# Performance work log

Measured on AMD Instinct MI355X. Metric: run time of the kernel, lower is better.

Reference implementation:

```python
import jax, jax.numpy as jnp
import numpy as np

B, N, D = 8, 512, 512
H = 8
DK = D // H  # 64 per-channel attention maps


def setup_inputs() -> dict:
    key = jax.random.key(0)
    k1, k2, k3 = jax.random.split(key, 3)
    inputs = jax.random.normal(k1, (B, N, D), dtype=jnp.float32)
    W_qkv = jax.random.normal(k2, (D, 3 * DK), dtype=jnp.float32) * 0.02
    W_o = jax.random.normal(k3, (DK, D), dtype=jnp.float32) * 0.02
    return {"inputs": inputs, "W_qkv": W_qkv, "W_o": W_o}


def reference(inputs, W_qkv, W_o):
    d_k = W_qkv.shape[1] // 3
    QKV = inputs @ W_qkv                      # (B, N, 3*d_k)
    Q = QKV[:, :, 0 * d_k:1 * d_k]
    K = QKV[:, :, 1 * d_k:2 * d_k]
    V = QKV[:, :, 2 * d_k:3 * d_k]
    scale = 1.0 / jnp.sqrt(jnp.asarray(d_k, dtype=QKV.dtype))
    # per-channel (head_dim=1) attention, batched over the d_k channels
    S = jnp.einsum('bnc,bmc->bcnm', Q, K) * scale   # (B, d_k, N, N)
    A = jax.nn.softmax(S, axis=-1)
    SA = jnp.einsum('bcnm,bmc->bnc', A, V)          # (B, N, d_k)
    return SA @ W_o                                 # (B, N, D)
```

## Files before the change

kernel.cpp:

```cpp
#include <hip/hip_runtime.h>
#include <math.h>

#define BB 8
#define NN 512
#define DD 512
#define DKK 64
#define NC 192
#define CHN (BB * DKK * NN)
#define XEL (BB * NN * DD)
#define WEL (NC * DD)
#define NFRAG_X (XEL / 8)
#define NFRAG_W (WEL / 8)
#define NJ 20

typedef short s8v   __attribute__((ext_vector_type(8)));
typedef float f32x4 __attribute__((ext_vector_type(4)));
typedef unsigned short ushort;

static __device__ __forceinline__ ushort bf16_rne(float f) {
    unsigned u = __float_as_uint(f);
    unsigned r = 0x7FFFu + ((u >> 16) & 1u);
    return (ushort)((u + r) >> 16);
}
static __device__ __forceinline__ float bf16_f32(ushort h) {
    return __uint_as_float(((unsigned)h) << 16);
}

__constant__ float c_invfact[NJ] = {
    1.0f, 1.0f, 0.5f, 1.6666667e-1f, 4.1666668e-2f, 8.3333338e-3f,
    1.3888889e-3f, 1.9841270e-4f, 2.4801588e-5f, 2.7557319e-6f,
    2.7557319e-7f, 2.5052108e-8f, 2.0876757e-9f, 1.6059044e-10f,
    1.1470746e-11f, 7.6471637e-13f, 4.7794773e-14f, 2.8114572e-15f,
    1.5619207e-16f, 8.2206352e-18f};

__global__ __launch_bounds__(256) void prep(const float* __restrict__ X,
                                            const float* __restrict__ W,
                                            ushort* __restrict__ Xfh,
                                            ushort* __restrict__ Xfl,
                                            ushort* __restrict__ Wfh,
                                            ushort* __restrict__ Wfl) {
    const int gtid = blockIdx.x * 256 + threadIdx.x;
    if (gtid < NFRAG_X) {
        const int st   = gtid >> 10;
        const int ks   = (gtid >> 6) & 15;
        const int lane = gtid & 63;
        const int lm   = lane & 15;
        const int quad = lane >> 4;
        const int row  = st * 16 + lm;
        const int k0   = ks * 32 + quad * 8;
        const float4 xa = *(const float4*)(X + (size_t)row * DD + k0);
        const float4 xb = *(const float4*)(X + (size_t)row * DD + k0 + 4);
        const float xe[8] = {xa.x, xa.y, xa.z, xa.w, xb.x, xb.y, xb.z, xb.w};
        s8v h, l;
        #pragma unroll
        for (int e = 0; e < 8; ++e) {
            const ushort hh = bf16_rne(xe[e]);
            h[e] = (short)hh;
            l[e] = (short)bf16_rne(xe[e] - bf16_f32(hh));
        }
        *(s8v*)(Xfh + (size_t)gtid * 8) = h;
        *(s8v*)(Xfl + (size_t)gtid * 8) = l;
    } else {
        const int widx = gtid - NFRAG_X;
        if (widx < NFRAG_W) {
            const int ct   = widx >> 10;
            const int ks   = (widx >> 6) & 15;
            const int lane = widx & 63;
            const int lm   = lane & 15;
            const int quad = lane >> 4;
            const int chan = ct * 16 + lm;
            const int k0   = ks * 32 + quad * 8;
            s8v h, l;
            #pragma unroll
            for (int e = 0; e < 8; ++e) {
                const float w = W[(size_t)(k0 + e) * NC + chan];
                const ushort hh = bf16_rne(w);
                h[e] = (short)hh;
                l[e] = (short)bf16_rne(w - bf16_f32(hh));
            }
            *(s8v*)(Wfh + (size_t)widx * 8) = h;
            *(s8v*)(Wfl + (size_t)widx * 8) = l;
        }
    }
}

__global__ __launch_bounds__(256) void qkv_mfma(const ushort* __restrict__ Xfh,
                                                const ushort* __restrict__ Xfl,
                                                const ushort* __restrict__ Wfh,
                                                const ushort* __restrict__ Wfl,
                                                float* __restrict__ qkv) {
    const int widx = blockIdx.x * 4 + (threadIdx.x >> 6);
    const int st   = widx / 12;
    const int ct   = widx - st * 12;
    const int lane = threadIdx.x & 63;

    const ushort* ax_h = Xfh + ((size_t)(st * 16) * 64 + lane) * 8;
    const ushort* ax_l = Xfl + ((size_t)(st * 16) * 64 + lane) * 8;
    const ushort* bw_h = Wfh + ((size_t)(ct * 16) * 64 + lane) * 8;
    const ushort* bw_l = Wfl + ((size_t)(ct * 16) * 64 + lane) * 8;

    f32x4 acc = {0.f, 0.f, 0.f, 0.f};

    #pragma unroll 4
    for (int ks = 0; ks < 16; ++ks) {
        const size_t off = (size_t)ks * 512;
        const s8v ah = *(const s8v*)(ax_h + off);
        const s8v al = *(const s8v*)(ax_l + off);
        const s8v bh = *(const s8v*)(bw_h + off);
        const s8v bl = *(const s8v*)(bw_l + off);
        acc = __builtin_amdgcn_mfma_f32_16x16x32_bf16(ah, bh, acc, 0, 0, 0);
        acc = __builtin_amdgcn_mfma_f32_16x16x32_bf16(ah, bl, acc, 0, 0, 0);
        acc = __builtin_amdgcn_mfma_f32_16x16x32_bf16(al, bh, acc, 0, 0, 0);
    }

    const int lm   = lane & 15;
    const int quad = lane >> 4;
    const int chan = ct * 16 + lm;
    const int which = chan >> 6;
    const int c     = chan & 63;
    const int seq0  = st * 16 + quad * 4;
    const int b     = seq0 >> 9;
    const int n0    = seq0 & 511;
    const float4 v = {acc[0], acc[1], acc[2], acc[3]};
    *(float4*)(qkv + (size_t)which * CHN + ((size_t)(b * DKK + c)) * NN + n0) = v;
}

__global__ __launch_bounds__(256) void attn_taylor(const float* __restrict__ qkv,
                                                   float* __restrict__ sa_t) {
    __shared__ float red[4][2 * NJ];
    __shared__ float coef[2 * NJ];

    const int tid = threadIdx.x;
    const size_t chan = (size_t)blockIdx.x * NN;
    const float* qp = qkv + chan;
    const float* kp = qkv + CHN + chan;
    const float* vp = qkv + 2 * CHN + chan;

    const float k0 = kp[tid], k1 = kp[tid + 256];
    const float v0 = vp[tid], v1 = vp[tid + 256];

    float m[2 * NJ];
    float p0 = 1.f, p1 = 1.f;
    #pragma unroll
    for (int j = 0; j < NJ; ++j) {
        m[j]      = fmaf(p0, v0, p1 * v1);
        m[NJ + j] = p0 + p1;
        p0 *= k0;
        p1 *= k1;
    }

    #pragma unroll
    for (int j = 0; j < 2 * NJ; ++j) {
        float s = m[j];
        #pragma unroll
        for (int off = 32; off > 0; off >>= 1)
            s += __shfl_down(s, off, 64);
        m[j] = s;
    }
    if ((tid & 63) == 0) {
        #pragma unroll
        for (int j = 0; j < 2 * NJ; ++j) red[tid >> 6][j] = m[j];
    }
    __syncthreads();
    if (tid < 2 * NJ) {
        const int jj = (tid < NJ) ? tid : tid - NJ;
        coef[tid] = (red[0][tid] + red[1][tid] + red[2][tid] + red[3][tid]) *
                    c_invfact[jj];
    }
    __syncthreads();

    float c[2 * NJ];
    #pragma unroll
    for (int j = 0; j < 2 * NJ; ++j) c[j] = coef[j];

    #pragma unroll
    for (int r = 0; r < 2; ++r) {
        const float t = qp[tid + r * 256] * 0.125f;
        float P = c[NJ - 1];
        float Q = c[2 * NJ - 1];
        #pragma unroll
        for (int j = NJ - 2; j >= 0; --j) {
            P = fmaf(P, t, c[j]);
            Q = fmaf(Q, t, c[NJ + j]);
        }
        sa_t[chan + tid + r * 256] = P / Q;
    }
}

__global__ __launch_bounds__(256) void out_gemm(const float* __restrict__ sa_t,
                                                const float* __restrict__ Wo,
                                                float* __restrict__ out) {
    __shared__ float As[64][68];
    __shared__ float Bs[64][68];

    const int tid  = threadIdx.x;
    const int row0 = blockIdx.x * 64;
    const int d0   = blockIdx.y * 64;
    const int b    = row0 >> 9;
    const int n0   = row0 & 511;

    const int f  = tid & 15;
    const int r0 = tid >> 4;
    #pragma unroll
    for (int rr = 0; rr < 4; ++rr) {
        const int cidx = r0 + rr * 16;
        *(float4*)&As[cidx][4 * f] =
            *(const float4*)(sa_t + (size_t)(b * DKK + cidx) * NN + n0 + 4 * f);
        *(float4*)&Bs[cidx][4 * f] =
            *(const float4*)(Wo + (size_t)cidx * DD + d0 + 4 * f);
    }
    __syncthreads();

    const int tc = tid & 15;
    const int tr = tid >> 4;
    float acc[4][4] = {};
    #pragma unroll 8
    for (int k = 0; k < DKK; ++k) {
        const float4 a  = *(const float4*)&As[k][4 * tr];
        const float4 bv = *(const float4*)&Bs[k][4 * tc];
        const float av[4] = {a.x, a.y, a.z, a.w};
        const float be[4] = {bv.x, bv.y, bv.z, bv.w};
        #pragma unroll
        for (int i = 0; i < 4; ++i)
            #pragma unroll
            for (int j = 0; j < 4; ++j)
                acc[i][j] = fmaf(av[i], be[j], acc[i][j]);
    }

    float* op = out + ((size_t)(b * NN + n0)) * DD + d0;
    #pragma unroll
    for (int i = 0; i < 4; ++i) {
        const float4 v = {acc[i][0], acc[i][1], acc[i][2], acc[i][3]};
        *(float4*)(op + (size_t)(4 * tr + i) * DD + 4 * tc) = v;
    }
}

extern "C" void kernel_launch(void* const* d_in, const int* in_sizes, int n_in,
                              void* d_out, int out_size, void* d_ws, size_t ws_size,
                              hipStream_t stream) {
    const float* X    = (const float*)d_in[0];
    const float* Wqkv = (const float*)d_in[1];
    const float* Wo   = (const float*)d_in[2];
    float* out = (float*)d_out;

    float*  qkv  = (float*)d_ws;
    float*  sa_t = qkv + (size_t)3 * CHN;
    ushort* Xfh  = (ushort*)(sa_t + CHN);
    ushort* Xfl  = Xfh + (size_t)XEL;
    ushort* Wfh  = Xfl + (size_t)XEL;
    ushort* Wfl  = Wfh + (size_t)WEL;

    prep<<<dim3((NFRAG_X + NFRAG_W + 255) / 256), 256, 0, stream>>>(
        X, Wqkv, Xfh, Xfl, Wfh, Wfl);
    qkv_mfma<<<dim3(768), 256, 0, stream>>>(Xfh, Xfl, Wfh, Wfl, qkv);
    attn_taylor<<<dim3(BB * DKK), 256, 0, stream>>>(qkv, sa_t);
    out_gemm<<<dim3(64, 8), 256, 0, stream>>>(sa_t, Wo, out);
}
```

Measured before the change: 89.91 us.

## Move output projection to split-bf16 MFMA and remap QKV blocks per XCD

The fp32 LDS-tiled output GEMM is replaced with an MFMA kernel using hi/lo bf16 splits (three products per k-step). The attention kernel now writes its result directly in the MFMA fragment layout, and W_o is converted to fragments in the prep kernel. The QKV GEMM block index is also remapped so each XCD handles a contiguous range of sequence tiles, which should improve L2 locality. In exchange, the attention kernel does scattered 2-byte stores, and the output kernel writes with a less coalesced pattern (per-lane scalar stores strided by DD).

```diff
diff --git a/kernel.cpp b/kernel.cpp
--- a/kernel.cpp
+++ b/kernel.cpp
@@ -9,8 +9,11 @@
 #define CHN (BB * DKK * NN)
 #define XEL (BB * NN * DD)
 #define WEL (NC * DD)
+#define WOEL (DKK * DD)
+#define SAEL (BB * NN * DKK)
 #define NFRAG_X (XEL / 8)
 #define NFRAG_W (WEL / 8)
+#define NFRAG_WO (WOEL / 8)
 #define NJ 20
 
 typedef short s8v   __attribute__((ext_vector_type(8)));
@@ -35,10 +38,13 @@
 
 __global__ __launch_bounds__(256) void prep(const float* __restrict__ X,
                                             const float* __restrict__ W,
+                                            const float* __restrict__ Wo,
                                             ushort* __restrict__ Xfh,
                                             ushort* __restrict__ Xfl,
                                             ushort* __restrict__ Wfh,
-                                            ushort* __restrict__ Wfl) {
+                                            ushort* __restrict__ Wfl,
+                                            ushort* __restrict__ Woh,
+                                            ushort* __restrict__ Wol) {
     const int gtid = blockIdx.x * 256 + threadIdx.x;
     if (gtid < NFRAG_X) {
         const int st   = gtid >> 10;
@@ -60,27 +66,48 @@
         }
         *(s8v*)(Xfh + (size_t)gtid * 8) = h;
         *(s8v*)(Xfl + (size_t)gtid * 8) = l;
-    } else {
-        const int widx = gtid - NFRAG_X;
-        if (widx < NFRAG_W) {
-            const int ct   = widx >> 10;
-            const int ks   = (widx >> 6) & 15;
-            const int lane = widx & 63;
-            const int lm   = lane & 15;
-            const int quad = lane >> 4;
-            const int chan = ct * 16 + lm;
-            const int k0   = ks * 32 + quad * 8;
-            s8v h, l;
-            #pragma unroll
-            for (int e = 0; e < 8; ++e) {
-                const float w = W[(size_t)(k0 + e) * NC + chan];
-                const ushort hh = bf16_rne(w);
-                h[e] = (short)hh;
-                l[e] = (short)bf16_rne(w - bf16_f32(hh));
-            }
-            *(s8v*)(Wfh + (size_t)widx * 8) = h;
-            *(s8v*)(Wfl + (size_t)widx * 8) = l;
+        return;
+    }
+    const int widx = gtid - NFRAG_X;
+    if (widx < NFRAG_W) {
+        const int ct   = widx >> 10;
+        const int ks   = (widx >> 6) & 15;
+        const int lane = widx & 63;
+        const int lm   = lane & 15;
+        const int quad = lane >> 4;
+        const int chan = ct * 16 + lm;
+        const int k0   = ks * 32 + quad * 8;
+        s8v h, l;
+        #pragma unroll
+        for (int e = 0; e < 8; ++e) {
+            const float w = W[(size_t)(k0 + e) * NC + chan];
+            const ushort hh = bf16_rne(w);
+            h[e] = (short)hh;
+            l[e] = (short)bf16_rne(w - bf16_f32(hh));
         }
+        *(s8v*)(Wfh + (size_t)widx * 8) = h;
+        *(s8v*)(Wfl + (size_t)widx * 8) = l;
+        return;
+    }
+    const int fi = widx - NFRAG_W;
+    if (fi < NFRAG_WO) {
+        const int lane = fi & 63;
+        const int ks   = (fi >> 6) & 1;
+        const int dt   = fi >> 7;
+        const int lm   = lane & 15;
+        const int quad = lane >> 4;
+        const int d    = dt * 16 + lm;
+        s8v h, l;
+        #pragma unroll
+        for (int e = 0; e < 8; ++e) {
+            const int c = ks * 32 + quad * 8 + e;
+            const float w = Wo[(size_t)c * DD + d];
+            const ushort hh = bf16_rne(w);
+            h[e] = (short)hh;
+            l[e] = (short)bf16_rne(w - bf16_f32(hh));
+        }
+        *(s8v*)(Woh + (size_t)fi * 8) = h;
+        *(s8v*)(Wol + (size_t)fi * 8) = l;
     }
 }
 
@@ -89,9 +116,12 @@
                                                 const ushort* __restrict__ Wfh,
                                                 const ushort* __restrict__ Wfl,
                                                 float* __restrict__ qkv) {
-    const int widx = blockIdx.x * 4 + (threadIdx.x >> 6);
-    const int st   = widx / 12;
-    const int ct   = widx - st * 12;
+    const int xcd  = blockIdx.x & 7;
+    const int grp  = blockIdx.x >> 3;
+    const int stl  = grp / 3;
+    const int part = grp - stl * 3;
+    const int st   = xcd * 32 + stl;
+    const int ct   = part * 4 + (threadIdx.x >> 6);
     const int lane = threadIdx.x & 63;
 
     const ushort* ax_h = Xfh + ((size_t)(st * 16) * 64 + lane) * 8;
@@ -113,9 +143,9 @@
         acc = __builtin_amdgcn_mfma_f32_16x16x32_bf16(al, bh, acc, 0, 0, 0);
     }
 
-    const int lm   = lane & 15;
-    const int quad = lane >> 4;
-    const int chan = ct * 16 + lm;
+    const int lm    = lane & 15;
+    const int quad  = lane >> 4;
+    const int chan  = ct * 16 + lm;
     const int which = chan >> 6;
     const int c     = chan & 63;
     const int seq0  = st * 16 + quad * 4;
@@ -126,7 +156,8 @@
 }
 
 __global__ __launch_bounds__(256) void attn_taylor(const float* __restrict__ qkv,
-                                                   float* __restrict__ sa_t) {
+                                                   ushort* __restrict__ SAh,
+                                                   ushort* __restrict__ SAl) {
     __shared__ float red[4][2 * NJ];
     __shared__ float coef[2 * NJ];
 
@@ -173,9 +204,16 @@
     #pragma unroll
     for (int j = 0; j < 2 * NJ; ++j) c[j] = coef[j];
 
+    const int b  = blockIdx.x >> 6;
+    const int ch = blockIdx.x & 63;
+    const int ks = ch >> 5;
+    const int jf = ch & 7;
+    const int lhi = ((ch & 31) >> 3) << 4;
+
     #pragma unroll
     for (int r = 0; r < 2; ++r) {
-        const float t = qp[tid + r * 256] * 0.125f;
+        const int n = tid + r * 256;
+        const float t = qp[n] * 0.125f;
         float P = c[NJ - 1];
         float Q = c[2 * NJ - 1];
         #pragma unroll
@@ -183,55 +221,61 @@
             P = fmaf(P, t, c[j]);
             Q = fmaf(Q, t, c[NJ + j]);
         }
-        sa_t[chan + tid + r * 256] = P / Q;
-    }
-}
-
-__global__ __launch_bounds__(256) void out_gemm(const float* __restrict__ sa_t,
-                                                const float* __restrict__ Wo,
+        const float val = P / Q;
+        const ushort hi = bf16_rne(val);
+        const ushort lo = bf16_rne(val - bf16_f32(hi));
+        const int gseq = b * NN + n;
+        const int st   = gseq >> 4;
+        const int lane = lhi | (gseq & 15);
+        const size_t addr = ((size_t)(st * 2 + ks) * 64 + lane) * 8 + jf;
+        SAh[addr] = hi;
+        SAl[addr] = lo;
+    }
+}
+
+__global__ __launch_bounds__(256) void out_mfma(const ushort* __restrict__ SAh,
+                                                const ushort* __restrict__ SAl,
+                                                const ushort* __restrict__ Woh,
+                                                const ushort* __restrict__ Wol,
                                                 float* __restrict__ out) {
-    __shared__ float As[64][68];
-    __shared__ float Bs[64][68];
-
-    const int tid  = threadIdx.x;
-    const int row0 = blockIdx.x * 64;
-    const int d0   = blockIdx.y * 64;
-    const int b    = row0 >> 9;
-    const int n0   = row0 & 511;
-
-    const int f  = tid & 15;
-    const int r0 = tid >> 4;
-    #pragma unroll
-    for (int rr = 0; rr < 4; ++rr) {
-        const int cidx = r0 + rr * 16;
-        *(float4*)&As[cidx][4 * f] =
-            *(const float4*)(sa_t + (size_t)(b * DKK + cidx) * NN + n0 + 4 * f);
-        *(float4*)&Bs[cidx][4 * f] =
-            *(const float4*)(Wo + (size_t)cidx * DD + d0 + 4 * f);
-    }
-    __syncthreads();
-
-    const int tc = tid & 15;
-    const int tr = tid >> 4;
-    float acc[4][4] = {};
-    #pragma unroll 8
-    for (int k = 0; k < DKK; ++k) {
-        const float4 a  = *(const float4*)&As[k][4 * tr];
-        const float4 bv = *(const float4*)&Bs[k][4 * tc];
-        const float av[4] = {a.x, a.y, a.z, a.w};
-        const float be[4] = {bv.x, bv.y, bv.z, bv.w};
-        #pragma unroll
-        for (int i = 0; i < 4; ++i)
-            #pragma unroll
-            for (int j = 0; j < 4; ++j)
-                acc[i][j] = fmaf(av[i], be[j], acc[i][j]);
-    }
-
-    float* op = out + ((size_t)(b * NN + n0)) * DD + d0;
-    #pragma unroll
-    for (int i = 0; i < 4; ++i) {
-        const float4 v = {acc[i][0], acc[i][1], acc[i][2], acc[i][3]};
-        *(float4*)(op + (size_t)(4 * tr + i) * DD + 4 * tc) = v;
+    const int widx = blockIdx.x * 4 + (threadIdx.x >> 6);
+    const int st   = widx >> 3;
+    const int dg   = widx & 7;
+    const int lane = threadIdx.x & 63;
+
+    const ushort* sa_h = SAh + ((size_t)(st * 2) * 64 + lane) * 8;
+    const ushort* sa_l = SAl + ((size_t)(st * 2) * 64 + lane) * 8;
+    const s8v ah0 = *(const s8v*)(sa_h);
+    const s8v ah1 = *(const s8v*)(sa_h + 512);
+    const s8v al0 = *(const s8v*)(sa_l);
+    const s8v al1 = *(const s8v*)(sa_l + 512);
+
+    const int lm   = lane & 15;
+    const int quad = lane >> 4;
+    const int seq0 = st * 16 + quad * 4;
+
+    #pragma unroll
+    for (int dti = 0; dti < 4; ++dti) {
+        const int dt = dg * 4 + dti;
+        const ushort* wo_h = Woh + ((size_t)(dt * 2) * 64 + lane) * 8;
+        const ushort* wo_l = Wol + ((size_t)(dt * 2) * 64 + lane) * 8;
+        const s8v bh0 = *(const s8v*)(wo_h);
+        const s8v bh1 = *(const s8v*)(wo_h + 512);
+        const s8v bl0 = *(const s8v*)(wo_l);
+        const s8v bl1 = *(const s8v*)(wo_l + 512);
+
+        f32x4 acc = {0.f, 0.f, 0.f, 0.f};
+        acc = __builtin_amdgcn_mfma_f32_16x16x32_bf16(ah0, bh0, acc, 0, 0, 0);
+        acc = __builtin_amdgcn_mfma_f32_16x16x32_bf16(ah0, bl0, acc, 0, 0, 0);
+        acc = __builtin_amdgcn_mfma_f32_16x16x32_bf16(al0, bh0, acc, 0, 0, 0);
+        acc = __builtin_amdgcn_mfma_f32_16x16x32_bf16(ah1, bh1, acc, 0, 0, 0);
+        acc = __builtin_amdgcn_mfma_f32_16x16x32_bf16(ah1, bl1, acc, 0, 0, 0);
+        acc = __builtin_amdgcn_mfma_f32_16x16x32_bf16(al1, bh1, acc, 0, 0, 0);
+
+        const int d = dt * 16 + lm;
+        #pragma unroll
+        for (int r = 0; r < 4; ++r)
+            out[(size_t)(seq0 + r) * DD + d] = acc[r];
     }
 }
 
@@ -243,16 +287,19 @@
     const float* Wo   = (const float*)d_in[2];
     float* out = (float*)d_out;
 
-    float*  qkv  = (float*)d_ws;
-    float*  sa_t = qkv + (size_t)3 * CHN;
-    ushort* Xfh  = (ushort*)(sa_t + CHN);
-    ushort* Xfl  = Xfh + (size_t)XEL;
-    ushort* Wfh  = Xfl + (size_t)XEL;
-    ushort* Wfl  = Wfh + (size_t)WEL;
-
-    prep<<<dim3((NFRAG_X + NFRAG_W + 255) / 256), 256, 0, stream>>>(
-        X, Wqkv, Xfh, Xfl, Wfh, Wfl);
+    float*  qkv = (float*)d_ws;
+    ushort* Xfh = (ushort*)(qkv + (size_t)3 * CHN);
+    ushort* Xfl = Xfh + (size_t)XEL;
+    ushort* Wfh = Xfl + (size_t)XEL;
+    ushort* Wfl = Wfh + (size_t)WEL;
+    ushort* Woh = Wfl + (size_t)WEL;
+    ushort* Wol = Woh + (size_t)WOEL;
+    ushort* SAh = Wol + (size_t)WOEL;
+    ushort* SAl = SAh + (size_t)SAEL;
+
+    prep<<<dim3((NFRAG_X + NFRAG_W + NFRAG_WO) / 256), 256, 0, stream>>>(
+        X, Wqkv, Wo, Xfh, Xfl, Wfh, Wfl, Woh, Wol);
     qkv_mfma<<<dim3(768), 256, 0, stream>>>(Xfh, Xfl, Wfh, Wfl, qkv);
-    attn_taylor<<<dim3(BB * DKK), 256, 0, stream>>>(qkv, sa_t);
-    out_gemm<<<dim3(64, 8), 256, 0, stream>>>(sa_t, Wo, out);
-}
+    attn_taylor<<<dim3(BB * DKK), 256, 0, stream>>>(qkv, SAh, SAl);
+    out_mfma<<<dim3(512), 256, 0, stream>>>(SAh, SAl, Woh, Wol, out);
+}
```

New measurement: 89.16 us. No clear change (-0.8%).
